# Kernel optimization log

Hardware: AMD Instinct MI355X
Metric: run time of the kernel (lower is better)

The kernel has to match this reference:

```python
import jax, jax.numpy as jnp
import numpy as np

BN_EPS = 1e-5


def setup_inputs() -> dict:
    key = jax.random.key(0)
    ks = jax.random.split(key, 8)
    B, T, D, Tu, Dout, M = 32, 4096, 128, 512, 64, 8
    feats = jax.random.normal(ks[0], (B, T, D), dtype=jnp.float32)
    # integer time-window ids stored in channel 0 of x; pin 0 and Tu-1 so
    # tw_uniq = arange(0, Tu) exactly (no -99 padding) for every batch row
    tw = jax.random.randint(ks[1], (B, T), 0, Tu)
    tw = tw.at[:, 0].set(0).at[:, 1].set(Tu - 1)
    x = jnp.concatenate([tw[..., None].astype(jnp.float32), feats], axis=-1)
    mask = jax.random.uniform(ks[2], (B, T, 1)) < 0.9
    mask = mask.at[:, :2].set(True)  # keep pinned min/max entries valid
    tw_uniq = jnp.broadcast_to(jnp.arange(Tu, dtype=jnp.float32)[None, :, None], (B, Tu, 1))
    bn_gamma = jax.random.uniform(ks[3], (D,), jnp.float32, 0.5, 1.5)
    bn_beta = 0.1 * jax.random.normal(ks[4], (D,), dtype=jnp.float32)
    bn_mean = jnp.zeros((D,), jnp.float32)
    bn_var = jnp.ones((D,), jnp.float32)
    conv_w = jax.random.normal(ks[5], (Dout, D), dtype=jnp.float32) / np.float32(np.sqrt(D))
    conv_b = jnp.zeros((Dout,), jnp.float32)
    fc_w = jax.random.normal(ks[6], (M, Dout), dtype=jnp.float32) / np.float32(np.sqrt(Dout))
    fc_b = jnp.zeros((M,), jnp.float32)
    return dict(x=x, mask=mask, tw_uniq=tw_uniq, bn_gamma=bn_gamma, bn_beta=bn_beta,
                bn_mean=bn_mean, bn_var=bn_var, conv_w=conv_w, conv_b=conv_b,
                fc_w=fc_w, fc_b=fc_b)


def reference(x, mask, tw_uniq, bn_gamma, bn_beta, bn_mean, bn_var,
              conv_w, conv_b, fc_w, fc_b):
    # --- TimeWindowPooling (segment-max form of the dense expand+where+amax) ---
    # torch computes amax_T(where(tw==tw_uniq & mask, x, 0)) -> max(0, group max).
    # Equivalent: scatter-max of mask-zeroed values into a zeros-initialized
    # (B, Tu, D) buffer, avoiding the O(B*T*Tu*D) blowup.
    tw = x[..., 0]           # (B, T) integer-valued, detached in torch
    feats = x[..., 1:]       # (B, T, D)
    B, T, D = feats.shape
    Tu = tw_uniq.shape[1]
    u0 = tw_uniq[:, 0, 0]    # per-batch window minimum
    idx = jnp.clip((tw - u0[:, None]).astype(jnp.int32), 0, Tu - 1)  # (B, T)
    vals = jnp.where(mask, feats, 0.0)  # masked rows contribute 0 == init value
    hidden = jnp.zeros((B, Tu, D), feats.dtype).at[jnp.arange(B)[:, None], idx].max(vals)
    # --- mlp_down: BatchNorm1d (inference stats) + 1x1 Conv1d over channels ---
    h = (hidden - bn_mean) * jax.lax.rsqrt(bn_var + BN_EPS) * bn_gamma + bn_beta
    h = jnp.einsum('bud,od->buo', h, conv_w) + conv_b  # (B, Tu, Dout)
    # --- fc_out ---
    return jnp.einsum('buo,mo->bum', h, fc_w) + fc_b   # (B, Tu, M)
```

## Files before the change

kernel.cpp:

```cpp
#include <hip/hip_runtime.h>

#define B_   32
#define T_   4096
#define D_   128
#define TU   512
#define M_   8
#define O_   64
#define DCH  16
#define NCH  8
#define PAD  17
#define BN_EPS 1e-5f
#define UB   4

typedef float f4u __attribute__((ext_vector_type(4), aligned(4)));

#define WS_STRIDE (B_ * TU * M_)

__global__ __launch_bounds__(1024) void fused_scatter_mm_kernel(
    const float* __restrict__ x,
    const int*   __restrict__ mask,
    const float* __restrict__ tw_uniq,
    const float* __restrict__ bn_gamma,
    const float* __restrict__ bn_beta,
    const float* __restrict__ bn_mean,
    const float* __restrict__ bn_var,
    const float* __restrict__ conv_w,
    const float* __restrict__ conv_b,
    const float* __restrict__ fc_w,
    const float* __restrict__ fc_b,
    float*       __restrict__ ws) {
    __shared__ unsigned hid[TU * PAD];
    __shared__ float wsm[M_ * DCH];
    __shared__ float tmp[M_ * DCH];
    __shared__ float biasc[M_];
    const int i = blockIdx.x;
    const int b = (i & 7) + 8 * ((i >> 3) & 3);
    const int c = i >> 5;
    const int tid = threadIdx.x;

    for (int p = tid; p < TU * PAD; p += 1024) hid[p] = 0u;
    if (tid < M_ * DCH) {
        const int m = tid >> 4, dl = tid & (DCH - 1), d = c * DCH + dl;
        float wraw = 0.f;
#pragma unroll
        for (int o = 0; o < O_; ++o) wraw += fc_w[m * O_ + o] * conv_w[o * D_ + d];
        const float sc = bn_gamma[d] * rsqrtf(bn_var[d] + BN_EPS);
        const float sh = bn_beta[d] - bn_mean[d] * sc;
        wsm[tid] = wraw * sc;
        tmp[tid] = wraw * sh;
    }
    __syncthreads();
    if (tid < M_) {
        float s = 0.f;
#pragma unroll
        for (int d = 0; d < DCH; ++d) s += tmp[tid * DCH + d];
        if (c == 0) {
            s += fc_b[tid];
            for (int o = 0; o < O_; ++o) s += fc_w[tid * O_ + o] * conv_b[o];
        }
        biasc[tid] = s;
    }

    const float* xb = x + (size_t)b * T_ * (D_ + 1);
    const int*   mb = mask + b * T_;
    const float  u0 = tw_uniq[b * TU];

    const int q = tid & 3;
    const int r = tid >> 2;
    for (int it = 0; it < T_ / 256 / UB; ++it) {
        f4u   fv[UB];
        float twf[UB];
        int   mk[UB];
#pragma unroll
        for (int j = 0; j < UB; ++j) {
            const int t = (it * UB + j) * 256 + r;
            const float* row = xb + (size_t)t * (D_ + 1);
            fv[j]  = *(const f4u*)(row + 1 + c * DCH + q * 4);
            twf[j] = row[0];
            mk[j]  = mb[t];
        }
#pragma unroll
        for (int j = 0; j < UB; ++j) {
            if (mk[j] != 0) {
                int u = min(max((int)(twf[j] - u0), 0), TU - 1);
                unsigned* hp = &hid[u * PAD + q * 4];
                if (fv[j].x > 0.0f) atomicMax(hp + 0, __float_as_uint(fv[j].x));
                if (fv[j].y > 0.0f) atomicMax(hp + 1, __float_as_uint(fv[j].y));
                if (fv[j].z > 0.0f) atomicMax(hp + 2, __float_as_uint(fv[j].z));
                if (fv[j].w > 0.0f) atomicMax(hp + 3, __float_as_uint(fv[j].w));
            }
        }
    }
    __syncthreads();

    const int u  = tid & (TU - 1);
    const int mh = tid >> 9;
    float a0 = biasc[mh * 4 + 0];
    float a1 = biasc[mh * 4 + 1];
    float a2 = biasc[mh * 4 + 2];
    float a3 = biasc[mh * 4 + 3];
#pragma unroll
    for (int d = 0; d < DCH; ++d) {
        float h = __uint_as_float(hid[u * PAD + d]);
        a0 += h * wsm[(mh * 4 + 0) * DCH + d];
        a1 += h * wsm[(mh * 4 + 1) * DCH + d];
        a2 += h * wsm[(mh * 4 + 2) * DCH + d];
        a3 += h * wsm[(mh * 4 + 3) * DCH + d];
    }
    float4 av = make_float4(a0, a1, a2, a3);
    float* wp = ws + (size_t)c * WS_STRIDE + ((size_t)(b * TU + u)) * M_ + mh * 4;
    *(float4*)wp = av;
}

__global__ __launch_bounds__(256) void reduce_kernel(
    const float* __restrict__ ws, float* __restrict__ out) {
    const int j = blockIdx.x;
    const int s = j >> 3;
    const int b = (j & 7) + 8 * (s & 3);
    const int uc = s >> 2;
    const int idx = (b * TU + uc * 32) * M_ + threadIdx.x;
    float acc = 0.f;
#pragma unroll
    for (int c = 0; c < NCH; ++c) acc += ws[(size_t)c * WS_STRIDE + idx];
    out[idx] = acc;
}

extern "C" void kernel_launch(void* const* d_in, const int* in_sizes, int n_in,
                              void* d_out, int out_size, void* d_ws, size_t ws_size,
                              hipStream_t stream) {
    const float* x        = (const float*)d_in[0];
    const int*   mask     = (const int*)  d_in[1];
    const float* tw_uniq  = (const float*)d_in[2];
    const float* bn_gamma = (const float*)d_in[3];
    const float* bn_beta  = (const float*)d_in[4];
    const float* bn_mean  = (const float*)d_in[5];
    const float* bn_var   = (const float*)d_in[6];
    const float* conv_w   = (const float*)d_in[7];
    const float* conv_b   = (const float*)d_in[8];
    const float* fc_w     = (const float*)d_in[9];
    const float* fc_b     = (const float*)d_in[10];
    float* ws  = (float*)d_ws;
    float* out = (float*)d_out;

    fused_scatter_mm_kernel<<<256, 1024, 0, stream>>>(
        x, mask, tw_uniq, bn_gamma, bn_beta, bn_mean, bn_var,
        conv_w, conv_b, fc_w, fc_b, ws);
    reduce_kernel<<<512, 256, 0, stream>>>(ws, out);
}
```

Baseline: 128.8 us.

## Stage scatter input rows through LDS via global_load_lds with one row per lane

Replaces the register-based row loads with per-wave asynchronous global-to-LDS copies (global_load_lds) of 64 rows per tile, including time-window ids and mask. Each lane now handles a whole row's 16-channel slice, so it computes the window index once and issues 16 atomics, instead of four lanes each doing 4. This is meant to cut VGPR pressure and address work, and to improve load efficiency. It adds about 72KB of per-wave staging LDS, which may hurt occupancy. It also drops the previous four-way unrolled load batching, so latency hiding per wave is reduced.

```diff
diff --git a/kernel.cpp b/kernel.cpp
--- a/kernel.cpp
+++ b/kernel.cpp
@@ -1,4 +1,5 @@
 #include <hip/hip_runtime.h>
+#include <stdint.h>
 
 #define B_   32
 #define T_   4096
@@ -8,13 +9,22 @@
 #define O_   64
 #define DCH  16
 #define NCH  8
+#define NP   NCH
 #define PAD  17
 #define BN_EPS 1e-5f
-#define UB   4
 
-typedef float f4u __attribute__((ext_vector_type(4), aligned(4)));
+#define NWAVE 16
+#define TROWS 64
+#define NTILE (T_ / (NWAVE * TROWS))
+
+#define HID_WORDS  (TU * PAD)
+#define WREG_WORDS 1152
+#define LDS_WORDS  (HID_WORDS + NWAVE * WREG_WORDS)
 
 #define WS_STRIDE (B_ * TU * M_)
+
+typedef const __attribute__((address_space(1))) void* gptr_t;
+typedef __attribute__((address_space(3))) void* lptr_t;
 
 __global__ __launch_bounds__(1024) void fused_scatter_mm_kernel(
     const float* __restrict__ x,
@@ -29,16 +39,16 @@
     const float* __restrict__ fc_w,
     const float* __restrict__ fc_b,
     float*       __restrict__ ws) {
-    __shared__ unsigned hid[TU * PAD];
+    __shared__ unsigned lds[LDS_WORDS];
     __shared__ float wsm[M_ * DCH];
     __shared__ float tmp[M_ * DCH];
     __shared__ float biasc[M_];
-    const int i = blockIdx.x;
-    const int b = (i & 7) + 8 * ((i >> 3) & 3);
-    const int c = i >> 5;
+    const int i   = blockIdx.x;
+    const int b   = (i & 7) + 8 * ((i >> 3) & 3);
+    const int c   = i >> 5;
     const int tid = threadIdx.x;
 
-    for (int p = tid; p < TU * PAD; p += 1024) hid[p] = 0u;
+    for (int p = tid; p < HID_WORDS; p += 1024) lds[p] = 0u;
     if (tid < M_ * DCH) {
         const int m = tid >> 4, dl = tid & (DCH - 1), d = c * DCH + dl;
         float wraw = 0.f;
@@ -65,29 +75,41 @@
     const int*   mb = mask + b * T_;
     const float  u0 = tw_uniq[b * TU];
 
-    const int q = tid & 3;
-    const int r = tid >> 2;
-    for (int it = 0; it < T_ / 256 / UB; ++it) {
-        f4u   fv[UB];
-        float twf[UB];
-        int   mk[UB];
+    const int w = tid >> 6;
+    const int l = tid & 63;
+    unsigned* wreg = &lds[HID_WORDS + w * WREG_WORDS];
+
+    for (int t = 0; t < NTILE; ++t) {
+        const int row = (t * NWAVE + w) * TROWS + l;
+        const float* rp = xb + (size_t)row * (D_ + 1);
+        asm volatile("" ::: "memory");
 #pragma unroll
-        for (int j = 0; j < UB; ++j) {
-            const int t = (it * UB + j) * 256 + r;
-            const float* row = xb + (size_t)t * (D_ + 1);
-            fv[j]  = *(const f4u*)(row + 1 + c * DCH + q * 4);
-            twf[j] = row[0];
-            mk[j]  = mb[t];
+        for (int k = 0; k < 4; ++k) {
+            __builtin_amdgcn_global_load_lds(
+                (gptr_t)(const void*)(rp + 1 + c * DCH + 4 * k),
+                (lptr_t)(void*)(wreg + k * 256), 16, 0, 0);
         }
+        __builtin_amdgcn_global_load_lds(
+            (gptr_t)(const void*)rp, (lptr_t)(void*)(wreg + 1024), 4, 0, 0);
+        __builtin_amdgcn_global_load_lds(
+            (gptr_t)(const void*)(mb + row), (lptr_t)(void*)(wreg + 1088), 4, 0, 0);
+        __builtin_amdgcn_s_waitcnt(0x0F70);
+        asm volatile("" ::: "memory");
+        float4 f[4];
 #pragma unroll
-        for (int j = 0; j < UB; ++j) {
-            if (mk[j] != 0) {
-                int u = min(max((int)(twf[j] - u0), 0), TU - 1);
-                unsigned* hp = &hid[u * PAD + q * 4];
-                if (fv[j].x > 0.0f) atomicMax(hp + 0, __float_as_uint(fv[j].x));
-                if (fv[j].y > 0.0f) atomicMax(hp + 1, __float_as_uint(fv[j].y));
-                if (fv[j].z > 0.0f) atomicMax(hp + 2, __float_as_uint(fv[j].z));
-                if (fv[j].w > 0.0f) atomicMax(hp + 3, __float_as_uint(fv[j].w));
+        for (int k = 0; k < 4; ++k)
+            f[k] = *(const float4*)&wreg[k * 256 + 4 * l];
+        const float twv = __uint_as_float(wreg[1024 + l]);
+        const int   mkv = (int)wreg[1088 + l];
+        if (mkv != 0) {
+            const int u = min(max((int)(twv - u0), 0), TU - 1);
+            unsigned* hp = &lds[u * PAD];
+#pragma unroll
+            for (int k = 0; k < 4; ++k) {
+                if (f[k].x > 0.0f) atomicMax(hp + 4 * k + 0, __float_as_uint(f[k].x));
+                if (f[k].y > 0.0f) atomicMax(hp + 4 * k + 1, __float_as_uint(f[k].y));
+                if (f[k].z > 0.0f) atomicMax(hp + 4 * k + 2, __float_as_uint(f[k].z));
+                if (f[k].w > 0.0f) atomicMax(hp + 4 * k + 3, __float_as_uint(f[k].w));
             }
         }
     }
@@ -101,11 +123,11 @@
     float a3 = biasc[mh * 4 + 3];
 #pragma unroll
     for (int d = 0; d < DCH; ++d) {
-        float h = __uint_as_float(hid[u * PAD + d]);
-        a0 += h * wsm[(mh * 4 + 0) * DCH + d];
-        a1 += h * wsm[(mh * 4 + 1) * DCH + d];
-        a2 += h * wsm[(mh * 4 + 2) * DCH + d];
-        a3 += h * wsm[(mh * 4 + 3) * DCH + d];
+        float hv = __uint_as_float(lds[u * PAD + d]);
+        a0 += hv * wsm[(mh * 4 + 0) * DCH + d];
+        a1 += hv * wsm[(mh * 4 + 1) * DCH + d];
+        a2 += hv * wsm[(mh * 4 + 2) * DCH + d];
+        a3 += hv * wsm[(mh * 4 + 3) * DCH + d];
     }
     float4 av = make_float4(a0, a1, a2, a3);
     float* wp = ws + (size_t)c * WS_STRIDE + ((size_t)(b * TU + u)) * M_ + mh * 4;
@@ -121,7 +143,7 @@
     const int idx = (b * TU + uc * 32) * M_ + threadIdx.x;
     float acc = 0.f;
 #pragma unroll
-    for (int c = 0; c < NCH; ++c) acc += ws[(size_t)c * WS_STRIDE + idx];
+    for (int p = 0; p < NP; ++p) acc += ws[(size_t)p * WS_STRIDE + idx];
     out[idx] = acc;
 }
 
```

Result: slower. 132.4 us (+2.9%).
